# Performance work log

Hardware: AMD Instinct MI355X
Metric: run time of the kernel (lower is better)

## Reference

```python
import jax, jax.numpy as jnp
import numpy as np

BS = 128          # block_size for weight scales
FP8_MAX = 448.0   # e4m3fn max


def setup_inputs() -> dict:
    key = jax.random.key(0)
    k1, k2, k3 = jax.random.split(key, 3)
    T, I, O = 8192, 4096, 6144  # tokens, input_size, output_size
    x = jax.random.normal(k1, (T, I), dtype=jnp.float32)
    # weight is stored as fp8 in the module; we generate fp32 and cast inside reference
    weight = jax.random.normal(k2, (O, I), dtype=jnp.float32) * 0.02
    weight_scale_inv = jax.random.uniform(k3, (O // BS, I // BS), dtype=jnp.float32,
                                          minval=0.5, maxval=1.5)
    return {"x": x, "weight": weight, "weight_scale_inv": weight_scale_inv}


def reference(x, weight, weight_scale_inv):
    # --- stored fp8 weight (module keeps weight in float8_e4m3fn) ---
    w_fp8 = weight.astype(jnp.float8_e4m3fn)
    O, I = w_fp8.shape
    # --- block-wise dequantization: W_deq[o,i] = w[o,i] * scale[o//BS, i//BS] ---
    w_deq = (w_fp8.astype(jnp.float32)
             .reshape(O // BS, BS, I // BS, BS)
             * weight_scale_inv[:, None, :, None]).reshape(O, I)
    # --- dynamic per-token fp8 quantization of activations ---
    amax = jnp.clip(jnp.max(jnp.abs(x), axis=-1, keepdims=True), 1e-12, None)
    x_scale = (amax / FP8_MAX).astype(jnp.float32)   # [T, 1]
    x_fp8 = (x / x_scale).astype(jnp.float8_e4m3fn)  # [T, I]
    # --- GEMM on dequantized operands: out = (x_fp8 * x_scale) @ W_deq^T ---
    out = (x_fp8.astype(jnp.float32) @ w_deq.T) * x_scale  # [T, O]
    return out
```

## Files before the change

### kernel.cpp

```cpp
#include <hip/hip_runtime.h>
#include <stdint.h>

#define T_TOK 8192
#define K_IN  4096
#define O_OUT 6144

typedef __attribute__((ext_vector_type(4))) float f32x4;
typedef __attribute__((ext_vector_type(8))) int i32x8;
typedef unsigned int uint32;


__device__ inline void load_lds_16(const void* g, void* l) {
    __builtin_amdgcn_global_load_lds(
        (const __attribute__((address_space(1))) unsigned int*)g,
        (__attribute__((address_space(3))) unsigned int*)l, 16, 0, 0);
}

__device__ inline int pack4_fp8(float a, float b, float c, float d) {
    int r = __builtin_amdgcn_cvt_pk_fp8_f32(a, b, 0, false);
    r = __builtin_amdgcn_cvt_pk_fp8_f32(c, d, r, true);
    return r;
}

__global__ __launch_bounds__(256) void quant_x(const float* __restrict__ x,
                                               uint32* __restrict__ xq,
                                               float* __restrict__ xscale) {
    const int t   = blockIdx.x;
    const int tid = threadIdx.x;
    const float4* row4 = (const float4*)(x + (size_t)t * K_IN);

    float4 v[4];
    float amax = 0.f;
#pragma unroll
    for (int j = 0; j < 4; ++j) {
        v[j] = row4[tid + j * 256];
        amax = fmaxf(amax, fmaxf(fmaxf(fabsf(v[j].x), fabsf(v[j].y)),
                                 fmaxf(fabsf(v[j].z), fabsf(v[j].w))));
    }
#pragma unroll
    for (int off = 32; off > 0; off >>= 1)
        amax = fmaxf(amax, __shfl_down(amax, off, 64));
    __shared__ float red[4];
    if ((tid & 63) == 0) red[tid >> 6] = amax;
    __syncthreads();
    amax = fmaxf(fmaxf(red[0], red[1]), fmaxf(red[2], red[3]));

    const float scale = fmaxf(amax, 1e-12f) / 448.0f;
    if (tid == 0) xscale[t] = scale;

    uint32* orow = xq + (size_t)t * (K_IN / 4);
#pragma unroll
    for (int j = 0; j < 4; ++j) {
        float q0 = v[j].x / scale, q1 = v[j].y / scale;
        float q2 = v[j].z / scale, q3 = v[j].w / scale;
        orow[tid + j * 256] = (uint32)pack4_fp8(q0, q1, q2, q3);
    }
}

__global__ __launch_bounds__(256) void quant_w(const float* __restrict__ w,
                                               uint32* __restrict__ wq) {
    const size_t u = (size_t)blockIdx.x * 256 + threadIdx.x;
    float4 v = ((const float4*)w)[u];
    wq[u] = (uint32)pack4_fp8(v.x, v.y, v.z, v.w);
}

__global__ __launch_bounds__(512, 2) void gemm_fp8(const unsigned char* __restrict__ A,
                                                   const unsigned char* __restrict__ B,
                                                   const float* __restrict__ sinv,
                                                   const float* __restrict__ xscale,
                                                   float* __restrict__ C) {
    constexpr int BM = 256, BN = 256, BK = 128;
    constexpr int NKB = K_IN / BK;
    extern __shared__ unsigned char smem[];

    const int bn  = blockIdx.x;
    const int bm  = blockIdx.y;
    const int tid = threadIdx.x;
    const int lane = tid & 63;
    const int wv   = tid >> 6;
    const int wm   = (wv >> 2) * 128;
    const int wn   = (wv & 3) * 64;
    const int G2   = (lane >> 4) * 2;

    const int tr = tid >> 3;
    const int kc = (tid & 7) ^ (tr & 7);
    const unsigned char* Ag = A + (size_t)(bm * BM + tr) * K_IN + kc * 16;
    const unsigned char* Bg = B + (size_t)(bn * BN + tr) * K_IN + kc * 16;
    const int ldst = tid * 16;

    const int rA  = lane & 15;
    const int sw  = lane & 7;
    const int cs0 = ((G2    ) ^ sw) * 16;
    const int cs1 = ((G2 | 1) ^ sw) * 16;

    const float* srow = sinv + (size_t)(bn * 2 + (wn >> 7)) * NKB;

    f32x4 acc[8][4] = {};
    float s_prev = srow[0];

#define STAGE_A(p_, k0_) {                                                   \
    unsigned char* d_ = smem + (p_) * 65536 + ldst;                          \
    _Pragma("unroll")                                                        \
    for (int s_ = 0; s_ < 4; ++s_)                                           \
        load_lds_16(Ag + (size_t)(s_ * 64) * K_IN + (k0_), d_ + s_ * 8192); }
#define STAGE_B(p_, k0_) {                                                   \
    unsigned char* d_ = smem + (p_) * 65536 + 32768 + ldst;                  \
    _Pragma("unroll")                                                        \
    for (int s_ = 0; s_ < 4; ++s_)                                           \
        load_lds_16(Bg + (size_t)(s_ * 64) * K_IN + (k0_), d_ + s_ * 8192); }

    union F { i32x8 v; int4 h[2]; };
    F a[4], b01[2], b23[2];

#define LDA(d_, i_) { const unsigned char* q_ = pA + (wm + (i_) * 16 + rA) * 128; \
    (d_).h[0] = *(const int4*)(q_ + cs0); (d_).h[1] = *(const int4*)(q_ + cs1); }
#define LDB(d_, j_) { const unsigned char* q_ = pB + (wn + (j_) * 16 + rA) * 128; \
    (d_).h[0] = *(const int4*)(q_ + cs0); (d_).h[1] = *(const int4*)(q_ + cs1); }
#define MFMA(i_, j_, af_, bf_)                                              \
    acc[i_][j_] = __builtin_amdgcn_mfma_scale_f32_16x16x128_f8f6f4(         \
        (af_).v, (bf_).v, acc[i_][j_], 0 , 0 ,            \
        0, 0x7f7f7f7f, 0, 0x7f7f7f7f);
#define WAIT_MFMA_PHASE() do {                                              \
    asm volatile("" ::: "memory");                                          \
    __builtin_amdgcn_s_barrier();                                           \
    asm volatile("s_waitcnt lgkmcnt(0)" ::: "memory");                      \
    __builtin_amdgcn_sched_barrier(0);                                      \
    __builtin_amdgcn_s_setprio(1); } while (0)
#define END_MFMA_PHASE() do {                                               \
    __builtin_amdgcn_s_setprio(0);                                          \
    asm volatile("" ::: "memory");                                          \
    __builtin_amdgcn_s_barrier();                                           \
    asm volatile("" ::: "memory"); } while (0)

    STAGE_A(0, 0); STAGE_B(0, 0);
    __syncthreads();

    for (int kb = 0; kb < NKB; ++kb) {
        const unsigned char* pA = smem + (kb & 1) * 65536;
        const unsigned char* pB = pA + 32768;
        const int  pn  = (kb & 1) ^ 1;
        const int  nk0 = (kb + 1) * BK;
        const bool pf  = (kb + 1) < NKB;
        const float s_cur = srow[kb];
        const float rr = s_prev / s_cur;
        s_prev = s_cur;

        if (pf) STAGE_A(pn, nk0);
        LDA(a[0], 0) LDA(a[1], 1) LDA(a[2], 2) LDA(a[3], 3)
        LDB(b01[0], 0) LDB(b01[1], 1)
#pragma unroll
        for (int i = 0; i < 4; ++i) { acc[i][0] *= rr; acc[i][1] *= rr; }
        WAIT_MFMA_PHASE();
#pragma unroll
        for (int i = 0; i < 4; ++i) { MFMA(i, 0, a[i], b01[0]); MFMA(i, 1, a[i], b01[1]); }
        END_MFMA_PHASE();

        if (pf) STAGE_B(pn, nk0);
        LDB(b23[0], 2) LDB(b23[1], 3)
#pragma unroll
        for (int i = 0; i < 4; ++i) { acc[i][2] *= rr; acc[i][3] *= rr; }
        WAIT_MFMA_PHASE();
#pragma unroll
        for (int i = 0; i < 4; ++i) { MFMA(i, 2, a[i], b23[0]); MFMA(i, 3, a[i], b23[1]); }
        END_MFMA_PHASE();

        LDA(a[0], 4) LDA(a[1], 5) LDA(a[2], 6) LDA(a[3], 7)
#pragma unroll
        for (int i = 0; i < 4; ++i) { acc[4 + i][2] *= rr; acc[4 + i][3] *= rr; }
        WAIT_MFMA_PHASE();
#pragma unroll
        for (int i = 0; i < 4; ++i) { MFMA(4 + i, 2, a[i], b23[0]); MFMA(4 + i, 3, a[i], b23[1]); }
        END_MFMA_PHASE();

        LDB(b01[0], 0) LDB(b01[1], 1)
#pragma unroll
        for (int i = 0; i < 4; ++i) { acc[4 + i][0] *= rr; acc[4 + i][1] *= rr; }
        WAIT_MFMA_PHASE();
#pragma unroll
        for (int i = 0; i < 4; ++i) { MFMA(4 + i, 0, a[i], b01[0]); MFMA(4 + i, 1, a[i], b01[1]); }
        __builtin_amdgcn_s_setprio(0);
        __syncthreads();
    }

#pragma unroll
    for (int i = 0; i < 8; ++i) {
#pragma unroll
        for (int r = 0; r < 4; ++r) {
            const int m_g = bm * BM + wm + i * 16 + (lane >> 4) * 4 + r;
            const float f = xscale[m_g] * s_prev;
            float* crow = C + (size_t)m_g * O_OUT + bn * BN + wn;
#pragma unroll
            for (int j = 0; j < 4; ++j)
                crow[j * 16 + (lane & 15)] = acc[i][j][r] * f;
        }
    }
#undef STAGE_A
#undef STAGE_B
#undef LDA
#undef LDB
#undef MFMA
#undef WAIT_MFMA_PHASE
#undef END_MFMA_PHASE
}

extern "C" void kernel_launch(void* const* d_in, const int* in_sizes, int n_in,
                              void* d_out, int out_size, void* d_ws, size_t ws_size,
                              hipStream_t stream) {
    const float* x    = (const float*)d_in[0];
    const float* w    = (const float*)d_in[1];
    const float* sinv = (const float*)d_in[2];
    float* out = (float*)d_out;

    char* ws = (char*)d_ws;
    uint32* xq = (uint32*)ws;
    uint32* wq = (uint32*)(ws + (size_t)T_TOK * K_IN);
    float* xscale = (float*)(ws + (size_t)T_TOK * K_IN
                                + (size_t)O_OUT * K_IN);

    quant_x<<<T_TOK, 256, 0, stream>>>(x, xq, xscale);
    quant_w<<<(O_OUT * K_IN) / (4 * 256), 256, 0, stream>>>(w, wq);
    dim3 grid(O_OUT / 256, T_TOK / 256);
    gemm_fp8<<<grid, 512, 131072 , stream>>>(
        (const unsigned char*)xq, (const unsigned char*)wq, sinv, xscale, out);
}
```

Measured before the change: 645.9 us.

## Load B fragments directly to registers and deepen A LDS pipeline to four stages

B tiles now skip LDS: each wave reads its weight fragments straight from global memory into registers, double-buffered across k-blocks. The freed LDS holds a four-stage ring for A, prefetched three blocks ahead. The four barrier-separated MFMA phases per k-block are merged into one loop with a single syncthreads. This aims to cut LDS traffic and barrier overhead and to hide more latency, at the cost of uncoalesced, uncached-in-LDS B global loads, more VGPRs, and stage prefetches that wrap around past the end of K.

```diff
diff --git a/kernel.cpp b/kernel.cpp
--- a/kernel.cpp
+++ b/kernel.cpp
@@ -85,101 +85,75 @@
     const int tr = tid >> 3;
     const int kc = (tid & 7) ^ (tr & 7);
     const unsigned char* Ag = A + (size_t)(bm * BM + tr) * K_IN + kc * 16;
-    const unsigned char* Bg = B + (size_t)(bn * BN + tr) * K_IN + kc * 16;
     const int ldst = tid * 16;
 
     const int rA  = lane & 15;
-    const int sw  = lane & 7;
-    const int cs0 = ((G2    ) ^ sw) * 16;
-    const int cs1 = ((G2 | 1) ^ sw) * 16;
+    const int cs0 = ((G2    ) ^ (lane & 7)) * 16;
+    const int cs1 = ((G2 + 1) ^ (lane & 7)) * 16;
+
+    const unsigned char* Bg = B + (size_t)(bn * BN + wn + rA) * K_IN + G2 * 16;
 
     const float* srow = sinv + (size_t)(bn * 2 + (wn >> 7)) * NKB;
 
+    union F { i32x8 v; int4 h[2]; };
     f32x4 acc[8][4] = {};
+    F bA[4], bB[4];
     float s_prev = srow[0];
 
-#define STAGE_A(p_, k0_) {                                                   \
-    unsigned char* d_ = smem + (p_) * 65536 + ldst;                          \
+#define STAGE(ck_) {                                                         \
+    unsigned char* d_ = smem + (size_t)((ck_) & 3) * 32768 + ldst;           \
+    const unsigned char* g_ = Ag + (size_t)((ck_) & 31) * BK;                \
+    load_lds_16(g_,                      d_);                                \
+    load_lds_16(g_ + (size_t) 64 * K_IN, d_ +  8192);                        \
+    load_lds_16(g_ + (size_t)128 * K_IN, d_ + 16384);                        \
+    load_lds_16(g_ + (size_t)192 * K_IN, d_ + 24576); }
+
+#define LOADB(dst_, ck_) {                                                   \
+    const unsigned char* g_ = Bg + (size_t)((ck_) & 31) * BK;                \
+    dst_[0].h[0] = *(const int4*)(g_);                                       \
+    dst_[0].h[1] = *(const int4*)(g_ + 16);                                  \
+    dst_[1].h[0] = *(const int4*)(g_ + (size_t)16 * K_IN);                   \
+    dst_[1].h[1] = *(const int4*)(g_ + (size_t)16 * K_IN + 16);              \
+    dst_[2].h[0] = *(const int4*)(g_ + (size_t)32 * K_IN);                   \
+    dst_[2].h[1] = *(const int4*)(g_ + (size_t)32 * K_IN + 16);              \
+    dst_[3].h[0] = *(const int4*)(g_ + (size_t)48 * K_IN);                   \
+    dst_[3].h[1] = *(const int4*)(g_ + (size_t)48 * K_IN + 16); }
+
+#define LDA(d_, i_, pA_) {                                                   \
+    const unsigned char* q_ = (pA_) + (wm + (i_) * 16 + rA) * 128;           \
+    (d_).h[0] = *(const int4*)(q_ + cs0);                                    \
+    (d_).h[1] = *(const int4*)(q_ + cs1); }
+
+#define MFMA(i_, j_, af_, bf_)                                               \
+    acc[i_][j_] = __builtin_amdgcn_mfma_scale_f32_16x16x128_f8f6f4(          \
+        (af_).v, (bf_).v, acc[i_][j_], 0 , 0 ,             \
+        0, 0x7f7f7f7f, 0, 0x7f7f7f7f);
+
+#define KB_BODY(kb_, bcur_, bnxt_) {                                         \
+    const unsigned char* pA = smem + (size_t)((kb_) & 3) * 32768;            \
+    const float s_cur = srow[kb_];                                           \
+    const float rr = s_prev / s_cur;               \
+    s_prev = s_cur;                                                          \
+    LOADB(bnxt_, (kb_) + 1);                                                 \
+    STAGE((kb_) + 3);                                                        \
+    __builtin_amdgcn_s_setprio(1);                                           \
     _Pragma("unroll")                                                        \
-    for (int s_ = 0; s_ < 4; ++s_)                                           \
-        load_lds_16(Ag + (size_t)(s_ * 64) * K_IN + (k0_), d_ + s_ * 8192); }
-#define STAGE_B(p_, k0_) {                                                   \
-    unsigned char* d_ = smem + (p_) * 65536 + 32768 + ldst;                  \
-    _Pragma("unroll")                                                        \
-    for (int s_ = 0; s_ < 4; ++s_)                                           \
-        load_lds_16(Bg + (size_t)(s_ * 64) * K_IN + (k0_), d_ + s_ * 8192); }
+    for (int i = 0; i < 8; ++i) {                                            \
+        F af; LDA(af, i, pA);                                                \
+        acc[i][0] *= rr; acc[i][1] *= rr; acc[i][2] *= rr; acc[i][3] *= rr;  \
+        MFMA(i, 0, af, bcur_[0]); MFMA(i, 1, af, bcur_[1]);                  \
+        MFMA(i, 2, af, bcur_[2]); MFMA(i, 3, af, bcur_[3]);                  \
+    }                                                                        \
+    __builtin_amdgcn_s_setprio(0);                                           \
+    __syncthreads(); }
 
-    union F { i32x8 v; int4 h[2]; };
-    F a[4], b01[2], b23[2];
-
-#define LDA(d_, i_) { const unsigned char* q_ = pA + (wm + (i_) * 16 + rA) * 128; \
-    (d_).h[0] = *(const int4*)(q_ + cs0); (d_).h[1] = *(const int4*)(q_ + cs1); }
-#define LDB(d_, j_) { const unsigned char* q_ = pB + (wn + (j_) * 16 + rA) * 128; \
-    (d_).h[0] = *(const int4*)(q_ + cs0); (d_).h[1] = *(const int4*)(q_ + cs1); }
-#define MFMA(i_, j_, af_, bf_)                                              \
-    acc[i_][j_] = __builtin_amdgcn_mfma_scale_f32_16x16x128_f8f6f4(         \
-        (af_).v, (bf_).v, acc[i_][j_], 0 , 0 ,            \
-        0, 0x7f7f7f7f, 0, 0x7f7f7f7f);
-#define WAIT_MFMA_PHASE() do {                                              \
-    asm volatile("" ::: "memory");                                          \
-    __builtin_amdgcn_s_barrier();                                           \
-    asm volatile("s_waitcnt lgkmcnt(0)" ::: "memory");                      \
-    __builtin_amdgcn_sched_barrier(0);                                      \
-    __builtin_amdgcn_s_setprio(1); } while (0)
-#define END_MFMA_PHASE() do {                                               \
-    __builtin_amdgcn_s_setprio(0);                                          \
-    asm volatile("" ::: "memory");                                          \
-    __builtin_amdgcn_s_barrier();                                           \
-    asm volatile("" ::: "memory"); } while (0)
-
-    STAGE_A(0, 0); STAGE_B(0, 0);
+    LOADB(bA, 0);
+    STAGE(0); STAGE(1); STAGE(2);
     __syncthreads();
 
-    for (int kb = 0; kb < NKB; ++kb) {
-        const unsigned char* pA = smem + (kb & 1) * 65536;
-        const unsigned char* pB = pA + 32768;
-        const int  pn  = (kb & 1) ^ 1;
-        const int  nk0 = (kb + 1) * BK;
-        const bool pf  = (kb + 1) < NKB;
-        const float s_cur = srow[kb];
-        const float rr = s_prev / s_cur;
-        s_prev = s_cur;
-
-        if (pf) STAGE_A(pn, nk0);
-        LDA(a[0], 0) LDA(a[1], 1) LDA(a[2], 2) LDA(a[3], 3)
-        LDB(b01[0], 0) LDB(b01[1], 1)
-#pragma unroll
-        for (int i = 0; i < 4; ++i) { acc[i][0] *= rr; acc[i][1] *= rr; }
-        WAIT_MFMA_PHASE();
-#pragma unroll
-        for (int i = 0; i < 4; ++i) { MFMA(i, 0, a[i], b01[0]); MFMA(i, 1, a[i], b01[1]); }
-        END_MFMA_PHASE();
-
-        if (pf) STAGE_B(pn, nk0);
-        LDB(b23[0], 2) LDB(b23[1], 3)
-#pragma unroll
-        for (int i = 0; i < 4; ++i) { acc[i][2] *= rr; acc[i][3] *= rr; }
-        WAIT_MFMA_PHASE();
-#pragma unroll
-        for (int i = 0; i < 4; ++i) { MFMA(i, 2, a[i], b23[0]); MFMA(i, 3, a[i], b23[1]); }
-        END_MFMA_PHASE();
-
-        LDA(a[0], 4) LDA(a[1], 5) LDA(a[2], 6) LDA(a[3], 7)
-#pragma unroll
-        for (int i = 0; i < 4; ++i) { acc[4 + i][2] *= rr; acc[4 + i][3] *= rr; }
-        WAIT_MFMA_PHASE();
-#pragma unroll
-        for (int i = 0; i < 4; ++i) { MFMA(4 + i, 2, a[i], b23[0]); MFMA(4 + i, 3, a[i], b23[1]); }
-        END_MFMA_PHASE();
-
-        LDB(b01[0], 0) LDB(b01[1], 1)
-#pragma unroll
-        for (int i = 0; i < 4; ++i) { acc[4 + i][0] *= rr; acc[4 + i][1] *= rr; }
-        WAIT_MFMA_PHASE();
-#pragma unroll
-        for (int i = 0; i < 4; ++i) { MFMA(4 + i, 0, a[i], b01[0]); MFMA(4 + i, 1, a[i], b01[1]); }
-        __builtin_amdgcn_s_setprio(0);
-        __syncthreads();
+    for (int kb = 0; kb < NKB; kb += 2) {
+        KB_BODY(kb,     bA, bB);
+        KB_BODY(kb + 1, bB, bA);
     }
 
 #pragma unroll
@@ -194,13 +168,11 @@
                 crow[j * 16 + (lane & 15)] = acc[i][j][r] * f;
         }
     }
-#undef STAGE_A
-#undef STAGE_B
+#undef STAGE
+#undef LOADB
 #undef LDA
-#undef LDB
 #undef MFMA
-#undef WAIT_MFMA_PHASE
-#undef END_MFMA_PHASE
+#undef KB_BODY
 }
 
 extern "C" void kernel_launch(void* const* d_in, const int* in_sizes, int n_in,
```

New measurement: 648.8 us. Within noise of the previous version (+0.5%).

## Interleave global-to-LDS prefetch across MFMA phases with fine-grained vmcnt waits

Applied to the files above, without the earlier changes.

The next K-tile's A and B global-to-LDS loads are now issued in pieces across the four MFMA phases of each iteration. Partial s_waitcnt vmcnt counts replace the full __syncthreads at the end of the loop, so memory traffic overlaps compute more evenly and the blocking drain per iteration goes away. The prefetch guard is removed: the last iteration wraps around and loads tile 0 again, which wastes some bandwidth but keeps the loop branch-free. The correctness of the vmcnt counts and the LDS buffer reuse depends on the new barrier placement.

```diff
diff --git a/kernel.cpp b/kernel.cpp
--- a/kernel.cpp
+++ b/kernel.cpp
@@ -85,102 +85,106 @@
     const int tr = tid >> 3;
     const int kc = (tid & 7) ^ (tr & 7);
     const unsigned char* Ag = A + (size_t)(bm * BM + tr) * K_IN + kc * 16;
-    const unsigned char* Bg = B + (size_t)(bn * BN + tr) * K_IN + kc * 16;
+    const unsigned char* Bgs = B + (size_t)(bn * BN + tr) * K_IN + kc * 16;
     const int ldst = tid * 16;
 
     const int rA  = lane & 15;
-    const int sw  = lane & 7;
-    const int cs0 = ((G2    ) ^ sw) * 16;
-    const int cs1 = ((G2 | 1) ^ sw) * 16;
+    const int cs0 = ((G2    ) ^ (lane & 7)) * 16;
+    const int cs1 = ((G2 + 1) ^ (lane & 7)) * 16;
 
     const float* srow = sinv + (size_t)(bn * 2 + (wn >> 7)) * NKB;
 
+    union F { i32x8 v; int4 h[2]; };
     f32x4 acc[8][4] = {};
+    F a[4], b0, b1, b2, b3;
     float s_prev = srow[0];
 
-#define STAGE_A(p_, k0_) {                                                   \
-    unsigned char* d_ = smem + (p_) * 65536 + ldst;                          \
-    _Pragma("unroll")                                                        \
-    for (int s_ = 0; s_ < 4; ++s_)                                           \
-        load_lds_16(Ag + (size_t)(s_ * 64) * K_IN + (k0_), d_ + s_ * 8192); }
-#define STAGE_B(p_, k0_) {                                                   \
-    unsigned char* d_ = smem + (p_) * 65536 + 32768 + ldst;                  \
-    _Pragma("unroll")                                                        \
-    for (int s_ = 0; s_ < 4; ++s_)                                           \
-        load_lds_16(Bg + (size_t)(s_ * 64) * K_IN + (k0_), d_ + s_ * 8192); }
-
-    union F { i32x8 v; int4 h[2]; };
-    F a[4], b01[2], b23[2];
-
-#define LDA(d_, i_) { const unsigned char* q_ = pA + (wm + (i_) * 16 + rA) * 128; \
+#define STG_A(p_, u_, k0_) load_lds_16(Ag + (size_t)(u_) * 64 * K_IN + (k0_), \
+        smem + (size_t)(p_) * 65536 + (u_) * 8192 + ldst)
+#define STG_B(p_, u_, k0_) load_lds_16(Bgs + (size_t)(u_) * 64 * K_IN + (k0_), \
+        smem + (size_t)(p_) * 65536 + 32768 + (u_) * 8192 + ldst)
+
+#define LDA_(d_, i_) { const unsigned char* q_ = pA + (wm + (i_) * 16 + rA) * 128; \
     (d_).h[0] = *(const int4*)(q_ + cs0); (d_).h[1] = *(const int4*)(q_ + cs1); }
-#define LDB(d_, j_) { const unsigned char* q_ = pB + (wn + (j_) * 16 + rA) * 128; \
+#define LDB_(d_, j_) { const unsigned char* q_ = pB + (wn + (j_) * 16 + rA) * 128; \
     (d_).h[0] = *(const int4*)(q_ + cs0); (d_).h[1] = *(const int4*)(q_ + cs1); }
-#define MFMA(i_, j_, af_, bf_)                                              \
-    acc[i_][j_] = __builtin_amdgcn_mfma_scale_f32_16x16x128_f8f6f4(         \
-        (af_).v, (bf_).v, acc[i_][j_], 0 , 0 ,            \
+
+#define MFMA(i_, j_, af_, bf_)                                               \
+    acc[i_][j_] = __builtin_amdgcn_mfma_scale_f32_16x16x128_f8f6f4(          \
+        (af_).v, (bf_).v, acc[i_][j_], 0 , 0 ,             \
         0, 0x7f7f7f7f, 0, 0x7f7f7f7f);
-#define WAIT_MFMA_PHASE() do {                                              \
-    asm volatile("" ::: "memory");                                          \
-    __builtin_amdgcn_s_barrier();                                           \
-    asm volatile("s_waitcnt lgkmcnt(0)" ::: "memory");                      \
-    __builtin_amdgcn_sched_barrier(0);                                      \
-    __builtin_amdgcn_s_setprio(1); } while (0)
-#define END_MFMA_PHASE() do {                                               \
-    __builtin_amdgcn_s_setprio(0);                                          \
-    asm volatile("" ::: "memory");                                          \
-    __builtin_amdgcn_s_barrier();                                           \
-    asm volatile("" ::: "memory"); } while (0)
-
-    STAGE_A(0, 0); STAGE_B(0, 0);
-    __syncthreads();
+
+#define FENCE() asm volatile("" ::: "memory")
+#define BARRIER() do { FENCE(); __builtin_amdgcn_s_barrier(); FENCE(); } while (0)
+#define VMW(n_) do { __builtin_amdgcn_sched_barrier(0);                      \
+    asm volatile("s_waitcnt vmcnt(" #n_ ")" ::: "memory");                   \
+    __builtin_amdgcn_sched_barrier(0); } while (0)
+#define LGKM0() do { asm volatile("s_waitcnt lgkmcnt(0)" ::: "memory");      \
+    __builtin_amdgcn_sched_barrier(0); } while (0)
+
+    STG_B(0, 0, 0); STG_B(0, 1, 0); STG_B(0, 2, 0); STG_B(0, 3, 0);
+    STG_A(0, 0, 0); STG_A(0, 2, 0);
+    STG_A(0, 1, 0); STG_A(0, 3, 0);
+    VMW(2);
+    BARRIER();
 
     for (int kb = 0; kb < NKB; ++kb) {
-        const unsigned char* pA = smem + (kb & 1) * 65536;
+        const unsigned char* pA = smem + (size_t)(kb & 1) * 65536;
         const unsigned char* pB = pA + 32768;
-        const int  pn  = (kb & 1) ^ 1;
-        const int  nk0 = (kb + 1) * BK;
-        const bool pf  = (kb + 1) < NKB;
+        const int    pn  = (kb + 1) & 1;
+        const size_t nk0 = (size_t)((kb + 1) & 31) * BK;
         const float s_cur = srow[kb];
         const float rr = s_prev / s_cur;
         s_prev = s_cur;
 
-        if (pf) STAGE_A(pn, nk0);
-        LDA(a[0], 0) LDA(a[1], 1) LDA(a[2], 2) LDA(a[3], 3)
-        LDB(b01[0], 0) LDB(b01[1], 1)
+        LDA_(a[0], 0) LDA_(a[1], 1) LDA_(a[2], 2) LDA_(a[3], 3)
+        LDB_(b0, 0) LDB_(b1, 1)
+        STG_B(pn, 0, nk0); STG_B(pn, 1, nk0);
 #pragma unroll
         for (int i = 0; i < 4; ++i) { acc[i][0] *= rr; acc[i][1] *= rr; }
-        WAIT_MFMA_PHASE();
-#pragma unroll
-        for (int i = 0; i < 4; ++i) { MFMA(i, 0, a[i], b01[0]); MFMA(i, 1, a[i], b01[1]); }
-        END_MFMA_PHASE();
-
-        if (pf) STAGE_B(pn, nk0);
-        LDB(b23[0], 2) LDB(b23[1], 3)
+        BARRIER(); LGKM0();
+        __builtin_amdgcn_s_setprio(1);
+#pragma unroll
+        for (int i = 0; i < 4; ++i) { MFMA(i, 0, a[i], b0); MFMA(i, 1, a[i], b1); }
+        __builtin_amdgcn_s_setprio(0);
+        BARRIER();
+
+        LDB_(b2, 2) LDB_(b3, 3)
+        STG_B(pn, 2, nk0); STG_B(pn, 3, nk0);
+        STG_A(pn, 0, nk0); STG_A(pn, 2, nk0);
 #pragma unroll
         for (int i = 0; i < 4; ++i) { acc[i][2] *= rr; acc[i][3] *= rr; }
-        WAIT_MFMA_PHASE();
-#pragma unroll
-        for (int i = 0; i < 4; ++i) { MFMA(i, 2, a[i], b23[0]); MFMA(i, 3, a[i], b23[1]); }
-        END_MFMA_PHASE();
-
-        LDA(a[0], 4) LDA(a[1], 5) LDA(a[2], 6) LDA(a[3], 7)
+        VMW(6);
+        BARRIER(); LGKM0();
+        __builtin_amdgcn_s_setprio(1);
+#pragma unroll
+        for (int i = 0; i < 4; ++i) { MFMA(i, 2, a[i], b2); MFMA(i, 3, a[i], b3); }
+        __builtin_amdgcn_s_setprio(0);
+        BARRIER();
+
+        LDA_(a[0], 4) LDA_(a[1], 5) LDA_(a[2], 6) LDA_(a[3], 7)
+        STG_A(pn, 1, nk0); STG_A(pn, 3, nk0);
 #pragma unroll
         for (int i = 0; i < 4; ++i) { acc[4 + i][2] *= rr; acc[4 + i][3] *= rr; }
-        WAIT_MFMA_PHASE();
-#pragma unroll
-        for (int i = 0; i < 4; ++i) { MFMA(4 + i, 2, a[i], b23[0]); MFMA(4 + i, 3, a[i], b23[1]); }
-        END_MFMA_PHASE();
-
-        LDB(b01[0], 0) LDB(b01[1], 1)
+        BARRIER(); LGKM0();
+        __builtin_amdgcn_s_setprio(1);
+#pragma unroll
+        for (int i = 0; i < 4; ++i) { MFMA(4 + i, 2, a[i], b2); MFMA(4 + i, 3, a[i], b3); }
+        __builtin_amdgcn_s_setprio(0);
+        BARRIER();
+
+        LDB_(b0, 0) LDB_(b1, 1)
 #pragma unroll
         for (int i = 0; i < 4; ++i) { acc[4 + i][0] *= rr; acc[4 + i][1] *= rr; }
-        WAIT_MFMA_PHASE();
-#pragma unroll
-        for (int i = 0; i < 4; ++i) { MFMA(4 + i, 0, a[i], b01[0]); MFMA(4 + i, 1, a[i], b01[1]); }
-        __builtin_amdgcn_s_setprio(0);
-        __syncthreads();
-    }
+        VMW(2);
+        BARRIER(); LGKM0();
+        __builtin_amdgcn_s_setprio(1);
+#pragma unroll
+        for (int i = 0; i < 4; ++i) { MFMA(4 + i, 0, a[i], b0); MFMA(4 + i, 1, a[i], b1); }
+        __builtin_amdgcn_s_setprio(0);
+        BARRIER();
+    }
+    VMW(0);
 
 #pragma unroll
     for (int i = 0; i < 8; ++i) {
@@ -194,13 +198,15 @@
                 crow[j * 16 + (lane & 15)] = acc[i][j][r] * f;
         }
     }
-#undef STAGE_A
-#undef STAGE_B
-#undef LDA
-#undef LDB
+#undef STG_A
+#undef STG_B
+#undef LDA_
+#undef LDB_
 #undef MFMA
-#undef WAIT_MFMA_PHASE
-#undef END_MFMA_PHASE
+#undef FENCE
+#undef BARRIER
+#undef VMW
+#undef LGKM0
 }
 
 extern "C" void kernel_launch(void* const* d_in, const int* in_sizes, int n_in,
```

After: 595.5 us. -7.8%, faster.
